# Optimization experiments

Measured on AMD Instinct MI355X. Metric: run time of the kernel, lower is better.

Reference implementation:

```python
import jax, jax.numpy as jnp
import numpy as np

LEAKY_SLOPE = 0.01  # torch F.leaky_relu default


def _l2norm(x):
    # matches F.normalize(p=2, dim=-1, eps=1e-12)
    n = jnp.linalg.norm(x, axis=-1, keepdims=True)
    return x / jnp.maximum(n, 1e-12)


def setup_inputs() -> dict:
    key = jax.random.key(0)
    k1, k2, k3, k4 = jax.random.split(key, 4)
    B, S, H = 16, 256, 768
    return {
        "query_embs": jax.random.normal(k1, (B, S, H), dtype=jnp.float32),
        "key_embs": jax.random.normal(k2, (2 * B, S, H), dtype=jnp.float32),
        "logit_scale": jnp.log(jnp.asarray(1.0 / 0.07, dtype=jnp.float32)),
        "alpha_raw": jnp.asarray(1.0, dtype=jnp.float32),
        "q_mask": jax.random.randint(k3, (B, S), 0, 2).astype(jnp.int32),
        "k_mask": jax.random.randint(k4, (2 * B, S), 0, 2).astype(jnp.int32),
    }


def reference(query_embs, key_embs, logit_scale, alpha_raw, q_mask, k_mask):
    q = _l2norm(query_embs)                 # [B, S, H]
    k = _l2norm(key_embs)                   # [2B, S, H]
    S = q.shape[1]

    # all-pairs token similarity: [B, 2B, S, S]
    sim = jnp.einsum('ish,jth->ijst', q, k)

    # exponential distance weighting
    pos = jnp.arange(S)
    dist = jnp.abs(pos[:, None] - pos[None, :]).astype(sim.dtype)
    alpha = jax.nn.leaky_relu(alpha_raw, LEAKY_SLOPE)
    sim = sim * jnp.exp(-alpha * dist)

    # joint validity mask: q_mask[i,s] & k_mask[j,t]
    valid = (q_mask[:, None, :, None] * k_mask[None, :, None, :]) > 0

    logits = jnp.where(valid, jnp.exp(logit_scale) * sim, -jnp.inf)
    p = jnp.nan_to_num(jax.nn.softmax(logits, axis=-1), nan=0.0)  # fully-masked rows -> 0

    # softmax-weighted aggregation of key tokens, then dot with query tokens
    agg = jnp.einsum('ijst,jth->ijsh', p, k)        # [B, 2B, S, H]
    per_tok = jnp.einsum('ish,ijsh->ijs', q, agg)   # [B, 2B, S]
    per_tok = per_tok * q_mask[:, None, :].astype(per_tok.dtype)
    return per_tok.sum(axis=-1)                     # [B, 2B]
```

## Files before the change

### kernel.cpp

```cpp
#include <hip/hip_runtime.h>
#include <hip/hip_bf16.h>

#define BQ   16
#define BK2  32
#define SEQ  256
#define HD   768

typedef __attribute__((ext_vector_type(8))) short bf16x8;
typedef __attribute__((ext_vector_type(4))) float f32x4;

__device__ __forceinline__ void glds16(const unsigned short* g, unsigned short* l) {
    __builtin_amdgcn_global_load_lds(
        (const __attribute__((address_space(1))) unsigned int*)g,
        (__attribute__((address_space(3))) unsigned int*)l, 16, 0, 0);
}

__device__ __forceinline__ unsigned int pack2_bf16(float a, float b) {
    unsigned ua = __float_as_uint(a), ub = __float_as_uint(b);
    ua += 0x7FFFu + ((ua >> 16) & 1u);
    ub += 0x7FFFu + ((ub >> 16) & 1u);
    return (ua >> 16) | (ub & 0xFFFF0000u);
}

__global__ __launch_bounds__(256) void norm_kernel(
    const float* __restrict__ q, const float* __restrict__ k,
    unsigned short* __restrict__ qn, unsigned short* __restrict__ kn,
    float* __restrict__ out)
{
    if (blockIdx.x == 0 && threadIdx.x < 256) {
        out[threadIdx.x] = 0.f; out[threadIdx.x + 256] = 0.f;
    }
    int row  = blockIdx.x * 4 + (threadIdx.x >> 6);
    int lane = threadIdx.x & 63;
    const int NQ = BQ * SEQ;
    const float* src = (row < NQ) ? q + (size_t)row * HD
                                  : k + (size_t)(row - NQ) * HD;
    unsigned int* dst = (unsigned int*)((row < NQ) ? qn + (size_t)row * HD
                                                   : kn + (size_t)(row - NQ) * HD);
    float4 v[3];
    float ss = 0.f;
#pragma unroll
    for (int c = 0; c < 3; ++c) {
        v[c] = ((const float4*)src)[lane + 64 * c];
        ss += v[c].x * v[c].x + v[c].y * v[c].y + v[c].z * v[c].z + v[c].w * v[c].w;
    }
#pragma unroll
    for (int m = 1; m < 64; m <<= 1) ss += __shfl_xor(ss, m, 64);
    float inv = rsqrtf(fmaxf(ss, 1e-24f));
#pragma unroll
    for (int c = 0; c < 3; ++c) {
        uint2 o = make_uint2(pack2_bf16(v[c].x * inv, v[c].y * inv),
                             pack2_bf16(v[c].z * inv, v[c].w * inv));
        ((uint2*)dst)[lane + 64 * c] = o;
    }
}

__global__ __launch_bounds__(512, 2) void li_kernel(
    const unsigned short* __restrict__ qn, const unsigned short* __restrict__ kn,
    const float* __restrict__ g_ls, const float* __restrict__ g_ar,
    const int* __restrict__ q_mask, const int* __restrict__ k_mask,
    float* __restrict__ out)
{
    const int j  = blockIdx.x, i = blockIdx.y, sh = blockIdx.z;
    const int tid  = threadIdx.x;
    const int w    = tid >> 6, lane = tid & 63;
    const int ln   = lane & 15, lg = lane >> 4;
    const int wsd  = w >> 2, wt = w & 3;

    __shared__ __align__(16) unsigned short As[128 * 64];
    __shared__ __align__(16) unsigned short Bs[256 * 64];
    __shared__ float w2[SEQ];
    __shared__ float kmB[SEQ];
    __shared__ float red[8];

    float a0 = g_ar[0];
    float alpha = (a0 > 0.f) ? a0 : 0.01f * a0;
    float scale = __expf(g_ls[0]) * 1.4426950408889634f;
    if (tid < 256) w2[tid] = scale * __expf(-alpha * (float)tid);
    else           kmB[tid - 256] = (k_mask[j * SEQ + (tid - 256)] != 0) ? 1.f : 0.f;

    const int rl  = lane >> 3;
    const int gch = (lane & 7) ^ rl;
    const unsigned short* aq = qn + ((size_t)i * SEQ + sh * 128 + w * 8 + rl) * HD + gch * 8;
    const unsigned short* bq = kn + ((size_t)j * SEQ + w * 8 + rl) * HD + gch * 8;
    unsigned short* al = As + (w * 8) * 64;
    unsigned short* bl = Bs + (w * 8) * 64;

    f32x4 acc[4][4];
    const f32x4 zero4 = {0.f, 0.f, 0.f, 0.f};
#pragma unroll
    for (int a = 0; a < 4; ++a)
#pragma unroll
        for (int b = 0; b < 4; ++b) acc[a][b] = zero4;

    for (int kk = 0; kk < HD; kk += 64) {
        __syncthreads();
        glds16(aq + kk,           al);
        glds16(aq + kk + 64 * HD, al + 64 * 64);
#pragma unroll
        for (int c = 0; c < 4; ++c)
            glds16(bq + kk + c * (64 * HD), bl + c * (64 * 64));
        __syncthreads();
        const bf16x8* A8 = (const bf16x8*)As;
        const bf16x8* B8 = (const bf16x8*)Bs;
#pragma unroll
        for (int ks = 0; ks < 2; ++ks) {
            const int ch = (ks * 4 + lg) ^ (ln & 7);
            bf16x8 af[4], bfr[4];
#pragma unroll
            for (int rm = 0; rm < 4; ++rm)
                af[rm] = A8[(wsd * 64 + rm * 16 + ln) * 8 + ch];
#pragma unroll
            for (int cn = 0; cn < 4; ++cn)
                bfr[cn] = B8[(wt * 64 + cn * 16 + ln) * 8 + ch];
#pragma unroll
            for (int rm = 0; rm < 4; ++rm)
#pragma unroll
                for (int cn = 0; cn < 4; ++cn)
                    acc[rm][cn] = __builtin_amdgcn_mfma_f32_16x16x32_bf16(
                        af[rm], bfr[cn], acc[rm][cn], 0, 0, 0);
        }
    }

    __syncthreads();
    float* zs  = (float*)Bs;
    float* wsc = zs + 16 * 132;

    float km[4];
#pragma unroll
    for (int cn = 0; cn < 4; ++cn) km[cn] = kmB[wt * 64 + cn * 16 + ln];

#pragma unroll
    for (int rm = 0; rm < 4; ++rm)
#pragma unroll
        for (int r = 0; r < 4; ++r) {
            int srow = wsd * 64 + rm * 16 + lg * 4 + r;
            int s  = sh * 128 + srow;
            float ze = 0.f, we = 0.f;
#pragma unroll
            for (int cn = 0; cn < 4; ++cn) {
                int t = wt * 64 + cn * 16 + ln;
                float sim = acc[rm][cn][r];
                int d = s - t; d = (d < 0) ? -d : d;
                float e = km[cn] * __builtin_exp2f(sim * w2[d]);
                ze += e;
                we = fmaf(e, sim, we);
            }
            ze += __shfl_xor(ze, 1, 64);  we += __shfl_xor(we, 1, 64);
            ze += __shfl_xor(ze, 2, 64);  we += __shfl_xor(we, 2, 64);
            if ((ln & 3) == 0) {
                int zrow = wt * 4 + (ln >> 2);
                zs [zrow * 132 + srow] = ze;
                wsc[zrow * 132 + srow] = we;
            }
        }
    __syncthreads();

    float part = 0.f;
    if (tid < 128) {
        float Z = 0.f, W = 0.f;
#pragma unroll
        for (int c = 0; c < 16; ++c) {
            Z += zs [c * 132 + tid];
            W += wsc[c * 132 + tid];
        }
        float pt = (Z > 0.f) ? (W / Z) : 0.f;
        part = pt * (float)q_mask[i * SEQ + sh * 128 + tid];
    }
#pragma unroll
    for (int m = 1; m < 64; m <<= 1) part += __shfl_xor(part, m, 64);
    if (lane == 0) red[w] = part;
    __syncthreads();
    if (tid == 0) {
        float tot = red[0] + red[1] + red[2] + red[3]
                  + red[4] + red[5] + red[6] + red[7];
        atomicAdd(&out[i * BK2 + j], tot);
    }
}

extern "C" void kernel_launch(void* const* d_in, const int* in_sizes, int n_in,
                              void* d_out, int out_size, void* d_ws, size_t ws_size,
                              hipStream_t stream) {
    const float* q  = (const float*)d_in[0];
    const float* k  = (const float*)d_in[1];
    const float* ls = (const float*)d_in[2];
    const float* ar = (const float*)d_in[3];
    const int* qm   = (const int*)d_in[4];
    const int* km   = (const int*)d_in[5];
    float* out      = (float*)d_out;

    unsigned short* qn = (unsigned short*)d_ws;
    unsigned short* kn = qn + (size_t)BQ * SEQ * HD;

    norm_kernel<<<(BQ + BK2) * SEQ / 4, 256, 0, stream>>>(q, k, qn, kn, (float*)d_out);
    li_kernel<<<dim3(BK2, BQ, 2), 512, 0, stream>>>(qn, kn, ls, ar, qm, km, (float*)d_out);
}
```

Baseline: 137.9 us.

## Compact masked query/key tokens and skip masked tiles in similarity GEMM

Adds a small kernel that compacts the valid-token indices of each query and key row using ballot/popcount. The main kernel then gathers only valid rows into LDS, exits early for query chunks with no valid tokens, and loops over only as many 128-wide key tiles as needed, accumulating the softmax partial sums across tiles. With random masks about half the tokens are valid, so this removes roughly half to three quarters of the MFMA and load work. In exchange it adds a third launch, per-row gathered global loads instead of contiguous ones, and a block shape of 256 threads with a 128x128 tile.

```diff
diff --git a/kernel.cpp b/kernel.cpp
--- a/kernel.cpp
+++ b/kernel.cpp
@@ -55,103 +55,163 @@
     }
 }
 
-__global__ __launch_bounds__(512, 2) void li_kernel(
+__global__ __launch_bounds__(64) void comp_kernel(
+    const int* __restrict__ q_mask, const int* __restrict__ k_mask,
+    int* __restrict__ sidx, int* __restrict__ cnts,
+    int* __restrict__ tidx, int* __restrict__ cntt)
+{
+    const int row  = blockIdx.x;
+    const int lane = threadIdx.x;
+    const bool isq = row < BQ;
+    const int* m = isq ? q_mask + row * SEQ : k_mask + (row - BQ) * SEQ;
+    int* idx     = isq ? sidx + row * SEQ  : tidx + (row - BQ) * SEQ;
+    int base = 0;
+#pragma unroll
+    for (int c = 0; c < 4; ++c) {
+        int v = (m[c * 64 + lane] != 0);
+        unsigned long long b = __ballot(v);
+        int pre = __popcll(b & ((1ull << lane) - 1ull));
+        if (v) idx[base + pre] = c * 64 + lane;
+        base += (int)__popcll(b);
+    }
+    for (int p = base + lane; p < SEQ; p += 64) idx[p] = 0;
+    if (lane == 0) { if (isq) cnts[row] = base; else cntt[row - BQ] = base; }
+}
+
+__global__ __launch_bounds__(256, 2) void li_kernel(
     const unsigned short* __restrict__ qn, const unsigned short* __restrict__ kn,
     const float* __restrict__ g_ls, const float* __restrict__ g_ar,
-    const int* __restrict__ q_mask, const int* __restrict__ k_mask,
+    const int* __restrict__ sidx, const int* __restrict__ cnts,
+    const int* __restrict__ tidx, const int* __restrict__ cntt,
     float* __restrict__ out)
 {
-    const int j  = blockIdx.x, i = blockIdx.y, sh = blockIdx.z;
+    const int j  = blockIdx.x, i = blockIdx.y, chs = blockIdx.z;
+    const int cs = cnts[i], ct = cntt[j];
+    if (chs * 128 >= cs) return;
+    const int nt = (ct + 127) >> 7;
+
     const int tid  = threadIdx.x;
     const int w    = tid >> 6, lane = tid & 63;
     const int ln   = lane & 15, lg = lane >> 4;
-    const int wsd  = w >> 2, wt = w & 3;
+    const int wsd  = w >> 1, wt = w & 1;
 
     __shared__ __align__(16) unsigned short As[128 * 64];
-    __shared__ __align__(16) unsigned short Bs[256 * 64];
+    __shared__ __align__(16) unsigned short Bs[128 * 64];
     __shared__ float w2[SEQ];
-    __shared__ float kmB[SEQ];
-    __shared__ float red[8];
+    __shared__ int   sor[128], tor[128];
+    __shared__ float red[4];
 
     float a0 = g_ar[0];
     float alpha = (a0 > 0.f) ? a0 : 0.01f * a0;
     float scale = __expf(g_ls[0]) * 1.4426950408889634f;
-    if (tid < 256) w2[tid] = scale * __expf(-alpha * (float)tid);
-    else           kmB[tid - 256] = (k_mask[j * SEQ + (tid - 256)] != 0) ? 1.f : 0.f;
-
-    const int rl  = lane >> 3;
-    const int gch = (lane & 7) ^ rl;
-    const unsigned short* aq = qn + ((size_t)i * SEQ + sh * 128 + w * 8 + rl) * HD + gch * 8;
-    const unsigned short* bq = kn + ((size_t)j * SEQ + w * 8 + rl) * HD + gch * 8;
-    unsigned short* al = As + (w * 8) * 64;
-    unsigned short* bl = Bs + (w * 8) * 64;
-
-    f32x4 acc[4][4];
-    const f32x4 zero4 = {0.f, 0.f, 0.f, 0.f};
+    w2[tid] = scale * __expf(-alpha * (float)tid);
+    if (tid < 128) sor[tid] = sidx[i * SEQ + chs * 128 + tid];
+
+    const int rw  = tid >> 3;
+    const int gch = (tid & 7) ^ (rw & 7);
+    int ia[4];
+#pragma unroll
+    for (int g = 0; g < 4; ++g)
+        ia[g] = sidx[i * SEQ + chs * 128 + g * 32 + rw];
+    const unsigned short* qb = qn + (size_t)i * SEQ * HD + gch * 8;
+    const unsigned short* kb = kn + (size_t)j * SEQ * HD + gch * 8;
+
+    float zeacc[4][4], weacc[4][4];
 #pragma unroll
     for (int a = 0; a < 4; ++a)
 #pragma unroll
-        for (int b = 0; b < 4; ++b) acc[a][b] = zero4;
-
-    for (int kk = 0; kk < HD; kk += 64) {
+        for (int b = 0; b < 4; ++b) { zeacc[a][b] = 0.f; weacc[a][b] = 0.f; }
+
+#pragma unroll 1
+    for (int tt = 0; tt < nt; ++tt) {
         __syncthreads();
-        glds16(aq + kk,           al);
-        glds16(aq + kk + 64 * HD, al + 64 * 64);
-#pragma unroll
-        for (int c = 0; c < 4; ++c)
-            glds16(bq + kk + c * (64 * HD), bl + c * (64 * 64));
-        __syncthreads();
-        const bf16x8* A8 = (const bf16x8*)As;
-        const bf16x8* B8 = (const bf16x8*)Bs;
-#pragma unroll
-        for (int ks = 0; ks < 2; ++ks) {
-            const int ch = (ks * 4 + lg) ^ (ln & 7);
-            bf16x8 af[4], bfr[4];
-#pragma unroll
-            for (int rm = 0; rm < 4; ++rm)
-                af[rm] = A8[(wsd * 64 + rm * 16 + ln) * 8 + ch];
-#pragma unroll
-            for (int cn = 0; cn < 4; ++cn)
-                bfr[cn] = B8[(wt * 64 + cn * 16 + ln) * 8 + ch];
-#pragma unroll
-            for (int rm = 0; rm < 4; ++rm)
+        if (tid < 128) tor[tid] = tidx[j * SEQ + tt * 128 + tid];
+        int ib[4];
+#pragma unroll
+        for (int g = 0; g < 4; ++g)
+            ib[g] = tidx[j * SEQ + tt * 128 + g * 32 + rw];
+
+        f32x4 acc[4][4];
+        const f32x4 zero4 = {0.f, 0.f, 0.f, 0.f};
+#pragma unroll
+        for (int a = 0; a < 4; ++a)
+#pragma unroll
+            for (int b = 0; b < 4; ++b) acc[a][b] = zero4;
+
+        for (int kk = 0; kk < HD; kk += 64) {
+            __syncthreads();
+#pragma unroll
+            for (int g = 0; g < 4; ++g) {
+                glds16(qb + (size_t)ia[g] * HD + kk, As + g * 2048 + w * 512);
+                glds16(kb + (size_t)ib[g] * HD + kk, Bs + g * 2048 + w * 512);
+            }
+            __syncthreads();
+            const bf16x8* A8 = (const bf16x8*)As;
+            const bf16x8* B8 = (const bf16x8*)Bs;
+#pragma unroll
+            for (int ks = 0; ks < 2; ++ks) {
+                const int ch = (ks * 4 + lg) ^ (ln & 7);
+                bf16x8 af[4], bfr[4];
+#pragma unroll
+                for (int rm = 0; rm < 4; ++rm)
+                    af[rm] = A8[(wsd * 64 + rm * 16 + ln) * 8 + ch];
 #pragma unroll
                 for (int cn = 0; cn < 4; ++cn)
-                    acc[rm][cn] = __builtin_amdgcn_mfma_f32_16x16x32_bf16(
-                        af[rm], bfr[cn], acc[rm][cn], 0, 0, 0);
-        }
+                    bfr[cn] = B8[(wt * 64 + cn * 16 + ln) * 8 + ch];
+#pragma unroll
+                for (int rm = 0; rm < 4; ++rm)
+#pragma unroll
+                    for (int cn = 0; cn < 4; ++cn)
+                        acc[rm][cn] = __builtin_amdgcn_mfma_f32_16x16x32_bf16(
+                            af[rm], bfr[cn], acc[rm][cn], 0, 0, 0);
+            }
+        }
+
+        const int ctrem = ct - tt * 128;
+        int   to[4];
+        float kv[4];
+#pragma unroll
+        for (int cn = 0; cn < 4; ++cn) {
+            int slot = wt * 64 + cn * 16 + ln;
+            to[cn] = tor[slot];
+            kv[cn] = (slot < ctrem) ? 1.f : 0.f;
+        }
+#pragma unroll
+        for (int rm = 0; rm < 4; ++rm)
+#pragma unroll
+            for (int r = 0; r < 4; ++r) {
+                int srow = wsd * 64 + rm * 16 + lg * 4 + r;
+                int so = sor[srow];
+                float ze = 0.f, we = 0.f;
+#pragma unroll
+                for (int cn = 0; cn < 4; ++cn) {
+                    float sim = acc[rm][cn][r];
+                    int d = so - to[cn]; d = (d < 0) ? -d : d;
+                    float e = kv[cn] * __builtin_exp2f(sim * w2[d]);
+                    ze += e;
+                    we = fmaf(e, sim, we);
+                }
+                zeacc[rm][r] += ze;
+                weacc[rm][r] += we;
+            }
     }
 
     __syncthreads();
-    float* zs  = (float*)Bs;
-    float* wsc = zs + 16 * 132;
-
-    float km[4];
-#pragma unroll
-    for (int cn = 0; cn < 4; ++cn) km[cn] = kmB[wt * 64 + cn * 16 + ln];
+    float* zs  = (float*)As;
+    float* wsc = zs + 8 * 133;
 
 #pragma unroll
     for (int rm = 0; rm < 4; ++rm)
 #pragma unroll
         for (int r = 0; r < 4; ++r) {
-            int srow = wsd * 64 + rm * 16 + lg * 4 + r;
-            int s  = sh * 128 + srow;
-            float ze = 0.f, we = 0.f;
-#pragma unroll
-            for (int cn = 0; cn < 4; ++cn) {
-                int t = wt * 64 + cn * 16 + ln;
-                float sim = acc[rm][cn][r];
-                int d = s - t; d = (d < 0) ? -d : d;
-                float e = km[cn] * __builtin_exp2f(sim * w2[d]);
-                ze += e;
-                we = fmaf(e, sim, we);
-            }
+            float ze = zeacc[rm][r], we = weacc[rm][r];
             ze += __shfl_xor(ze, 1, 64);  we += __shfl_xor(we, 1, 64);
             ze += __shfl_xor(ze, 2, 64);  we += __shfl_xor(we, 2, 64);
             if ((ln & 3) == 0) {
+                int srow = wsd * 64 + rm * 16 + lg * 4 + r;
                 int zrow = wt * 4 + (ln >> 2);
-                zs [zrow * 132 + srow] = ze;
-                wsc[zrow * 132 + srow] = we;
+                zs [zrow * 133 + srow] = ze;
+                wsc[zrow * 133 + srow] = we;
             }
         }
     __syncthreads();
@@ -160,22 +220,19 @@
     if (tid < 128) {
         float Z = 0.f, W = 0.f;
 #pragma unroll
-        for (int c = 0; c < 16; ++c) {
-            Z += zs [c * 132 + tid];
-            W += wsc[c * 132 + tid];
+        for (int c = 0; c < 8; ++c) {
+            Z += zs [c * 133 + tid];
+            W += wsc[c * 133 + tid];
         }
         float pt = (Z > 0.f) ? (W / Z) : 0.f;
-        part = pt * (float)q_mask[i * SEQ + sh * 128 + tid];
+        part = (chs * 128 + tid < cs) ? pt : 0.f;
     }
 #pragma unroll
     for (int m = 1; m < 64; m <<= 1) part += __shfl_xor(part, m, 64);
     if (lane == 0) red[w] = part;
     __syncthreads();
-    if (tid == 0) {
-        float tot = red[0] + red[1] + red[2] + red[3]
-                  + red[4] + red[5] + red[6] + red[7];
-        atomicAdd(&out[i * BK2 + j], tot);
-    }
+    if (tid == 0)
+        atomicAdd(&out[i * BK2 + j], red[0] + red[1] + red[2] + red[3]);
 }
 
 extern "C" void kernel_launch(void* const* d_in, const int* in_sizes, int n_in,
@@ -191,7 +248,14 @@
 
     unsigned short* qn = (unsigned short*)d_ws;
     unsigned short* kn = qn + (size_t)BQ * SEQ * HD;
+    int* sidx = (int*)(kn + (size_t)BK2 * SEQ * HD);
+    int* cnts = sidx + BQ * SEQ;
+    int* tidx = cnts + BQ;
+    int* cntt = tidx + BK2 * SEQ;
 
     norm_kernel<<<(BQ + BK2) * SEQ / 4, 256, 0, stream>>>(q, k, qn, kn, (float*)d_out);
-    li_kernel<<<dim3(BK2, BQ, 2), 512, 0, stream>>>(qn, kn, ls, ar, qm, km, (float*)d_out);
-}
+    comp_kernel<<<BQ + BK2, 64, 0, stream>>>(qm, km, sidx, cnts, tidx, cntt);
+    li_kernel<<<dim3(BK2, BQ, 2), 256, 0, stream>>>(qn, kn, ls, ar,
+                                                    sidx, cnts, tidx, cntt,
+                                                    (float*)d_out);
+}
```

After: 154.0 us. 1.12x slower.
